# Performance work log

Hardware: AMD Instinct MI355X
Metric: run time of the kernel (lower is better)

## Reference

```python
import jax, jax.numpy as jnp
import numpy as np

N_NODES = 100000
N_EDGES = 3200000
D = 64


def setup_inputs() -> dict:
    key = jax.random.key(0)
    ks = jax.random.split(key, 8)
    x = jax.random.normal(ks[0], (N_NODES, D), dtype=jnp.float32)
    adj_row = jnp.sort(jax.random.randint(ks[1], (N_EDGES,), 0, N_NODES, dtype=jnp.int32)).astype(jnp.int64)
    adj_col = jax.random.randint(ks[2], (N_EDGES,), 0, N_NODES, dtype=jnp.int32).astype(jnp.int64)
    adj_val = jax.random.uniform(ks[3], (N_EDGES,), dtype=jnp.float32)
    stdv = 1.0 / np.sqrt(D)
    W1 = jax.random.uniform(ks[4], (D, D), minval=-stdv, maxval=stdv, dtype=jnp.float32)
    b1 = jax.random.uniform(ks[5], (D,), minval=-stdv, maxval=stdv, dtype=jnp.float32)
    W2 = jax.random.uniform(ks[6], (D, D), minval=-stdv, maxval=stdv, dtype=jnp.float32)
    b2 = jax.random.uniform(ks[7], (D,), minval=-stdv, maxval=stdv, dtype=jnp.float32)
    return {"x": x, "adj_row": adj_row, "adj_col": adj_col, "adj_val": adj_val,
            "W1": W1, "b1": b1, "W2": W2, "b2": b2}


def _spmm(row, col, val, support):
    # output[i] = sum_{e: row[e]==i} val[e] * support[col[e]]  (COO SpMM)
    return jax.ops.segment_sum(val[:, None] * support[col], row, num_segments=N_NODES)


def _gc_layer(x, row, col, val, W, b):
    support = x @ W            # dense mm [N, D]
    out = _spmm(row, col, val, support)
    return out + b


def reference(x, adj_row, adj_col, adj_val, W1, b1, W2, b2):
    # layer 0 + LeakyReLU(0.2)
    h = _gc_layer(x, adj_row, adj_col, adj_val, W1, b1)
    h = jnp.where(h >= 0, h, 0.2 * h)
    # dropout is identity in eval mode
    # layer 1 (no activation)
    out = _gc_layer(h, adj_row, adj_col, adj_val, W2, b2)
    return out
```

## Files before the change

kernel.cpp:

```cpp
#include <hip/hip_runtime.h>

#define NN 100000
#define NE 3200000
#define DD 64
#define KE 64
#define NW (NE / KE)
#define GEMM_BLOCKS 391
#define PREP_BLOCKS 12501

typedef unsigned int uint32;

__device__ inline uint32 bf16_rne(float f) {
    uint32 u = __float_as_uint(f);
    return (u + 0x7fffu + ((u >> 16) & 1u)) >> 16;
}

__global__ __launch_bounds__(256) void pre_kernel(
    const void* rowbuf, const void* colbuf, const float* __restrict__ val,
    const float* __restrict__ x, const float* __restrict__ W1,
    uint32* __restrict__ erec, int* __restrict__ rp, int* __restrict__ ws,
    uint32* __restrict__ xw) {
    __shared__ float4 sW[DD * 16];

    if (blockIdx.x < GEMM_BLOCKS) {
        for (int i = threadIdx.x; i < DD * 16; i += 256)
            sW[i] = ((const float4*)W1)[i];
        __syncthreads();

        int row = blockIdx.x * 256 + threadIdx.x;
        if (row >= NN) return;

        float acc[DD];
#pragma unroll
        for (int j = 0; j < DD; ++j) acc[j] = 0.f;

        const float4* Bp = (const float4*)(x + (size_t)row * DD);
#pragma unroll
        for (int k4 = 0; k4 < 16; ++k4) {
            float4 x4 = Bp[k4];
            float xs[4] = {x4.x, x4.y, x4.z, x4.w};
#pragma unroll
            for (int kk = 0; kk < 4; ++kk) {
                float xk = xs[kk];
                int k = 4 * k4 + kk;
#pragma unroll
                for (int j4 = 0; j4 < 16; ++j4) {
                    float4 w = sW[k * 16 + j4];
                    acc[4 * j4 + 0] = fmaf(xk, w.x, acc[4 * j4 + 0]);
                    acc[4 * j4 + 1] = fmaf(xk, w.y, acc[4 * j4 + 1]);
                    acc[4 * j4 + 2] = fmaf(xk, w.z, acc[4 * j4 + 2]);
                    acc[4 * j4 + 3] = fmaf(xk, w.w, acc[4 * j4 + 3]);
                }
            }
        }
        uint32* o = xw + (size_t)row * 32;
#pragma unroll
        for (int q = 0; q < 32; ++q)
            o[q] = bf16_rne(acc[2 * q]) | (bf16_rne(acc[2 * q + 1]) << 16);
        return;
    }

    int e = (blockIdx.x - GEMM_BLOCKS) * 256 + threadIdx.x;
    if (e >= NE + 32) return;
    if (e >= NE) { erec[e] = 0u; return; }

    const int* p32 = (const int*)rowbuf;
    bool is64 = (p32[NE / 2 + 1] == 0 && p32[NE / 2] != 0);

    int r, rn, c;
    if (is64) {
        const long long* row = (const long long*)rowbuf;
        const long long* col = (const long long*)colbuf;
        r  = (int)row[e];
        rn = (e == NE - 1) ? NN : (int)row[e + 1];
        c  = (int)col[e];
    } else {
        const int* row = (const int*)rowbuf;
        const int* col = (const int*)colbuf;
        r  = row[e];
        rn = (e == NE - 1) ? NN : row[e + 1];
        c  = col[e];
    }
    erec[e] = ((bf16_rne(val[e]) & 0x7fffu) << 17) | (uint32)c;
    for (int q = r + 1; q <= rn; ++q) rp[q] = e + 1;
    if (e == 0) {
        for (int q = 0; q <= r; ++q) rp[q] = 0;
        ws[0]  = 0;
        ws[NW] = NN;
    }
    if (((e + 1) & (KE - 1)) == 0 && (e + 1) < NE)
        ws[(e + 1) / KE] = r + 1;
}

#define ISSUE(G, U, I) {                                        \
    U = (uint32)__shfl((int)rw, (I), 16);                       \
    G = ((const uint2*)Xq)[((U & 0x1ffffu) << 4) + sl]; }

#define FLUSH() {                                                       \
    float y0 = a0 + bv.x, y1 = a1 + bv.y,                               \
          y2 = a2 + bv.z, y3 = a3 + bv.w;                               \
    if (L1) {                                                           \
        y0 = (y0 >= 0.f) ? y0 : 0.2f * y0;                              \
        y1 = (y1 >= 0.f) ? y1 : 0.2f * y1;                              \
        y2 = (y2 >= 0.f) ? y2 : 0.2f * y2;                              \
        y3 = (y3 >= 0.f) ? y3 : 0.2f * y3;                              \
        unsigned long long pk =                                         \
            (unsigned long long)(bf16_rne(y0) | (bf16_rne(y1) << 16)) | \
            ((unsigned long long)(bf16_rne(y2) | (bf16_rne(y3) << 16)) << 32); \
        __builtin_nontemporal_store(pk,                                 \
            (unsigned long long*)((uint2*)obv + (size_t)rr * 16 + sl)); \
    } else {                                                            \
        float* op = (float*)obv + (size_t)rr * 64 + sl * 4;             \
        __builtin_nontemporal_store(y0, op);                            \
        __builtin_nontemporal_store(y1, op + 1);                        \
        __builtin_nontemporal_store(y2, op + 2);                        \
        __builtin_nontemporal_store(y3, op + 3);                        \
    }                                                                   \
    a0 = 0.f; a1 = 0.f; a2 = 0.f; a3 = 0.f; ++rr; }

#define ACCUM(G, U, I) {                                        \
    while (e0 + (I) >= re) {                                    \
        FLUSH();                                                \
        re = (rr < r1) ? rp[rr + 1] : 0x7fffffff;               \
    }                                                           \
    float vi_ = __uint_as_float((U >> 17) << 16);               \
    a0 = fmaf(vi_, __uint_as_float(G.x << 16),          a0);    \
    a1 = fmaf(vi_, __uint_as_float(G.x & 0xffff0000u),  a1);    \
    a2 = fmaf(vi_, __uint_as_float(G.y << 16),          a2);    \
    a3 = fmaf(vi_, __uint_as_float(G.y & 0xffff0000u),  a3); }

template <bool L1>
__global__ __launch_bounds__(256) void spmm_kernel(
    const uint32* __restrict__ Xq, const uint32* __restrict__ erec,
    const int* __restrict__ rp, const int* __restrict__ ws,
    const float* __restrict__ bias, void* __restrict__ obv) {
    int worker = (blockIdx.x * blockDim.x + threadIdx.x) >> 4;
    int sl = threadIdx.x & 15;
    if (worker >= NW) return;

    int rr = ws[worker];
    int r1 = ws[worker + 1];
    if (rr >= r1) return;

    const float4 bv = ((const float4*)bias)[sl];

    int eb = rp[rr];
    int ee = rp[r1];
    int re = rp[rr + 1];
    float a0 = 0.f, a1 = 0.f, a2 = 0.f, a3 = 0.f;

    for (int e0 = eb; e0 < ee; e0 += 16) {
        uint32 rw = __builtin_nontemporal_load(&erec[e0 + sl]);
        rw = (e0 + sl < ee) ? rw : 0u;
        uint2  g0, g1, g2, g3, g4, g5, g6, g7;
        uint2  h0, h1, h2, h3, h4, h5, h6, h7;
        uint32 u0, u1, u2, u3, u4, u5, u6, u7;
        uint32 w0, w1, w2, w3, w4, w5, w6, w7;
        ISSUE(g0, u0, 0)  ISSUE(g1, u1, 1)  ISSUE(g2, u2, 2)  ISSUE(g3, u3, 3)
        ISSUE(g4, u4, 4)  ISSUE(g5, u5, 5)  ISSUE(g6, u6, 6)  ISSUE(g7, u7, 7)
        ISSUE(h0, w0, 8)  ISSUE(h1, w1, 9)  ISSUE(h2, w2, 10) ISSUE(h3, w3, 11)
        ISSUE(h4, w4, 12) ISSUE(h5, w5, 13) ISSUE(h6, w6, 14) ISSUE(h7, w7, 15)
        ACCUM(g0, u0, 0)  ACCUM(g1, u1, 1)  ACCUM(g2, u2, 2)  ACCUM(g3, u3, 3)
        ACCUM(g4, u4, 4)  ACCUM(g5, u5, 5)  ACCUM(g6, u6, 6)  ACCUM(g7, u7, 7)
        ACCUM(h0, w0, 8)  ACCUM(h1, w1, 9)  ACCUM(h2, w2, 10) ACCUM(h3, w3, 11)
        ACCUM(h4, w4, 12) ACCUM(h5, w5, 13) ACCUM(h6, w6, 14) ACCUM(h7, w7, 15)
    }
    while (rr < r1) { FLUSH(); }
}

__global__ __launch_bounds__(256) void gemm_bb_kernel(
    const uint32* __restrict__ Bb, const float* __restrict__ W,
    uint32* __restrict__ ob) {
    __shared__ float4 sW[DD * 16];
    for (int i = threadIdx.x; i < DD * 16; i += 256)
        sW[i] = ((const float4*)W)[i];
    __syncthreads();

    int row = blockIdx.x * 256 + threadIdx.x;
    if (row >= NN) return;

    float acc[DD];
#pragma unroll
    for (int j = 0; j < DD; ++j) acc[j] = 0.f;

    const uint4* Bp = (const uint4*)(Bb + (size_t)row * 32);
#pragma unroll
    for (int q4 = 0; q4 < 8; ++q4) {
        uint4 u4 = Bp[q4];
        uint32 us[4] = {u4.x, u4.y, u4.z, u4.w};
#pragma unroll
        for (int t = 0; t < 4; ++t) {
            int k = q4 * 8 + t * 2;
            float x0 = __uint_as_float(us[t] << 16);
            float x1 = __uint_as_float(us[t] & 0xffff0000u);
#pragma unroll
            for (int j4 = 0; j4 < 16; ++j4) {
                float4 w0 = sW[k * 16 + j4];
                float4 w1 = sW[(k + 1) * 16 + j4];
                acc[4 * j4 + 0] = fmaf(x0, w0.x, acc[4 * j4 + 0]);
                acc[4 * j4 + 1] = fmaf(x0, w0.y, acc[4 * j4 + 1]);
                acc[4 * j4 + 2] = fmaf(x0, w0.z, acc[4 * j4 + 2]);
                acc[4 * j4 + 3] = fmaf(x0, w0.w, acc[4 * j4 + 3]);
                acc[4 * j4 + 0] = fmaf(x1, w1.x, acc[4 * j4 + 0]);
                acc[4 * j4 + 1] = fmaf(x1, w1.y, acc[4 * j4 + 1]);
                acc[4 * j4 + 2] = fmaf(x1, w1.z, acc[4 * j4 + 2]);
                acc[4 * j4 + 3] = fmaf(x1, w1.w, acc[4 * j4 + 3]);
            }
        }
    }

    uint32* o = ob + (size_t)row * 32;
#pragma unroll
    for (int q = 0; q < 32; ++q)
        o[q] = bf16_rne(acc[2 * q]) | (bf16_rne(acc[2 * q + 1]) << 16);
}

extern "C" void kernel_launch(void* const* d_in, const int* in_sizes, int n_in,
                              void* d_out, int out_size, void* d_ws, size_t ws_size,
                              hipStream_t stream) {
    const float* x       = (const float*)d_in[0];
    const void*  adj_row = d_in[1];
    const void*  adj_col = d_in[2];
    const float* adj_val = (const float*)d_in[3];
    const float* W1      = (const float*)d_in[4];
    const float* b1      = (const float*)d_in[5];
    const float* W2      = (const float*)d_in[6];
    const float* b2      = (const float*)d_in[7];
    float*       out     = (float*)d_out;

    uint32* bufA = (uint32*)d_ws;
    uint32* bufB = bufA + (size_t)NN * 32;
    uint32* erec = bufB + (size_t)NN * 32;
    int*    rp   = (int*)(erec + NE + 32);
    int*    wst  = rp + (NN + 1);

    const int spmm_blocks = (NW * 16) / 256;

    pre_kernel<<<GEMM_BLOCKS + PREP_BLOCKS, 256, 0, stream>>>(
        adj_row, adj_col, adj_val, x, W1, erec, rp, wst, bufB);

    spmm_kernel<true><<<spmm_blocks, 256, 0, stream>>>(bufB, erec, rp, wst,
                                                       b1, bufA);

    gemm_bb_kernel<<<GEMM_BLOCKS, 256, 0, stream>>>(bufA, W2, bufB);

    spmm_kernel<false><<<spmm_blocks, 256, 0, stream>>>(bufB, erec, rp, wst,
                                                        b2, out);
}
```

Baseline: 222.3 us.

## Quantize gathered feature rows to int8 with per-row scale

Replaces the bf16 packed intermediate features with uint8 (offset-128) per-row quantized values plus a float scale per row. The SpMM gathers 64-byte rows and a scale, and corrects the offset via an accumulated sum of weights at flush. The intent is to halve the random gather traffic, which dominates the SpMM. In exchange it adds quantization error, an extra scale load per edge, and issues loads in two batches of eight instead of sixteen.

```diff
diff --git a/kernel.cpp b/kernel.cpp
--- a/kernel.cpp
+++ b/kernel.cpp
@@ -15,11 +15,30 @@
     return (u + 0x7fffu + ((u >> 16) & 1u)) >> 16;
 }
 
+__device__ inline void quant_store(const float* acc, uint32* __restrict__ qrow,
+                                   float* __restrict__ scp) {
+    float m = 0.f;
+#pragma unroll
+    for (int j = 0; j < DD; ++j) m = fmaxf(m, fabsf(acc[j]));
+    float inv = (m > 0.f) ? (127.f / m) : 0.f;
+    *scp = m * (1.f / 127.f);
+#pragma unroll
+    for (int q = 0; q < 16; ++q) {
+        uint32 p = 0;
+#pragma unroll
+        for (int b = 0; b < 4; ++b) {
+            int v = (int)rintf(acc[4 * q + b] * inv) + 128;
+            p |= ((uint32)v) << (8 * b);
+        }
+        qrow[q] = p;
+    }
+}
+
 __global__ __launch_bounds__(256) void pre_kernel(
     const void* rowbuf, const void* colbuf, const float* __restrict__ val,
     const float* __restrict__ x, const float* __restrict__ W1,
     uint32* __restrict__ erec, int* __restrict__ rp, int* __restrict__ ws,
-    uint32* __restrict__ xw) {
+    uint32* __restrict__ qt, float* __restrict__ sc) {
     __shared__ float4 sW[DD * 16];
 
     if (blockIdx.x < GEMM_BLOCKS) {
@@ -53,10 +72,7 @@
                 }
             }
         }
-        uint32* o = xw + (size_t)row * 32;
-#pragma unroll
-        for (int q = 0; q < 32; ++q)
-            o[q] = bf16_rne(acc[2 * q]) | (bf16_rne(acc[2 * q + 1]) << 16);
+        quant_store(acc, qt + (size_t)row * 16, sc + row);
         return;
     }
 
@@ -92,13 +108,17 @@
         ws[(e + 1) / KE] = r + 1;
 }
 
-#define ISSUE(G, U, I) {                                        \
-    U = (uint32)__shfl((int)rw, (I), 16);                       \
-    G = ((const uint2*)Xq)[((U & 0x1ffffu) << 4) + sl]; }
+#define ISSUE(G, S, V, I) {                                     \
+    uint32 t_ = (uint32)__shfl((int)rw, (I), 16);               \
+    uint32 c_ = t_ & 0x1ffffu;                                  \
+    G = qt[((size_t)c_ << 4) + (uint32)sl];                     \
+    S = sc[c_];                                                 \
+    V = __uint_as_float((t_ >> 17) << 16); }
 
 #define FLUSH() {                                                       \
-    float y0 = a0 + bv.x, y1 = a1 + bv.y,                               \
-          y2 = a2 + bv.z, y3 = a3 + bv.w;                               \
+    float cr_ = fmaf(-128.f, ts, 0.f);                                  \
+    float y0 = a0 + cr_ + bv.x, y1 = a1 + cr_ + bv.y,                   \
+          y2 = a2 + cr_ + bv.z, y3 = a3 + cr_ + bv.w;                   \
     if (L1) {                                                           \
         y0 = (y0 >= 0.f) ? y0 : 0.2f * y0;                              \
         y1 = (y1 >= 0.f) ? y1 : 0.2f * y1;                              \
@@ -116,24 +136,26 @@
         __builtin_nontemporal_store(y2, op + 2);                        \
         __builtin_nontemporal_store(y3, op + 3);                        \
     }                                                                   \
-    a0 = 0.f; a1 = 0.f; a2 = 0.f; a3 = 0.f; ++rr; }
-
-#define ACCUM(G, U, I) {                                        \
+    a0 = 0.f; a1 = 0.f; a2 = 0.f; a3 = 0.f; ts = 0.f; ++rr; }
+
+#define ACCUM(G, S, V, I) {                                     \
     while (e0 + (I) >= re) {                                    \
         FLUSH();                                                \
         re = (rr < r1) ? rp[rr + 1] : 0x7fffffff;               \
     }                                                           \
-    float vi_ = __uint_as_float((U >> 17) << 16);               \
-    a0 = fmaf(vi_, __uint_as_float(G.x << 16),          a0);    \
-    a1 = fmaf(vi_, __uint_as_float(G.x & 0xffff0000u),  a1);    \
-    a2 = fmaf(vi_, __uint_as_float(G.y << 16),          a2);    \
-    a3 = fmaf(vi_, __uint_as_float(G.y & 0xffff0000u),  a3); }
+    float t_ = V * S;                                           \
+    a0 = fmaf(t_, (float)(G & 0xffu),         a0);              \
+    a1 = fmaf(t_, (float)((G >> 8) & 0xffu),  a1);              \
+    a2 = fmaf(t_, (float)((G >> 16) & 0xffu), a2);              \
+    a3 = fmaf(t_, (float)(G >> 24),           a3);              \
+    ts += t_; }
 
 template <bool L1>
 __global__ __launch_bounds__(256) void spmm_kernel(
-    const uint32* __restrict__ Xq, const uint32* __restrict__ erec,
-    const int* __restrict__ rp, const int* __restrict__ ws,
-    const float* __restrict__ bias, void* __restrict__ obv) {
+    const uint32* __restrict__ qt, const float* __restrict__ sc,
+    const uint32* __restrict__ erec, const int* __restrict__ rp,
+    const int* __restrict__ ws, const float* __restrict__ bias,
+    void* __restrict__ obv) {
     int worker = (blockIdx.x * blockDim.x + threadIdx.x) >> 4;
     int sl = threadIdx.x & 15;
     if (worker >= NW) return;
@@ -147,30 +169,37 @@
     int eb = rp[rr];
     int ee = rp[r1];
     int re = rp[rr + 1];
-    float a0 = 0.f, a1 = 0.f, a2 = 0.f, a3 = 0.f;
+    float a0 = 0.f, a1 = 0.f, a2 = 0.f, a3 = 0.f, ts = 0.f;
 
     for (int e0 = eb; e0 < ee; e0 += 16) {
         uint32 rw = __builtin_nontemporal_load(&erec[e0 + sl]);
         rw = (e0 + sl < ee) ? rw : 0u;
-        uint2  g0, g1, g2, g3, g4, g5, g6, g7;
-        uint2  h0, h1, h2, h3, h4, h5, h6, h7;
-        uint32 u0, u1, u2, u3, u4, u5, u6, u7;
-        uint32 w0, w1, w2, w3, w4, w5, w6, w7;
-        ISSUE(g0, u0, 0)  ISSUE(g1, u1, 1)  ISSUE(g2, u2, 2)  ISSUE(g3, u3, 3)
-        ISSUE(g4, u4, 4)  ISSUE(g5, u5, 5)  ISSUE(g6, u6, 6)  ISSUE(g7, u7, 7)
-        ISSUE(h0, w0, 8)  ISSUE(h1, w1, 9)  ISSUE(h2, w2, 10) ISSUE(h3, w3, 11)
-        ISSUE(h4, w4, 12) ISSUE(h5, w5, 13) ISSUE(h6, w6, 14) ISSUE(h7, w7, 15)
-        ACCUM(g0, u0, 0)  ACCUM(g1, u1, 1)  ACCUM(g2, u2, 2)  ACCUM(g3, u3, 3)
-        ACCUM(g4, u4, 4)  ACCUM(g5, u5, 5)  ACCUM(g6, u6, 6)  ACCUM(g7, u7, 7)
-        ACCUM(h0, w0, 8)  ACCUM(h1, w1, 9)  ACCUM(h2, w2, 10) ACCUM(h3, w3, 11)
-        ACCUM(h4, w4, 12) ACCUM(h5, w5, 13) ACCUM(h6, w6, 14) ACCUM(h7, w7, 15)
+        uint32 g0, g1, g2, g3, g4, g5, g6, g7;
+        float  s0, s1, s2, s3, s4, s5, s6, s7;
+        float  v0, v1, v2, v3, v4, v5, v6, v7;
+        ISSUE(g0, s0, v0, 0)  ISSUE(g1, s1, v1, 1)
+        ISSUE(g2, s2, v2, 2)  ISSUE(g3, s3, v3, 3)
+        ISSUE(g4, s4, v4, 4)  ISSUE(g5, s5, v5, 5)
+        ISSUE(g6, s6, v6, 6)  ISSUE(g7, s7, v7, 7)
+        ACCUM(g0, s0, v0, 0)  ACCUM(g1, s1, v1, 1)
+        ACCUM(g2, s2, v2, 2)  ACCUM(g3, s3, v3, 3)
+        ACCUM(g4, s4, v4, 4)  ACCUM(g5, s5, v5, 5)
+        ACCUM(g6, s6, v6, 6)  ACCUM(g7, s7, v7, 7)
+        ISSUE(g0, s0, v0, 8)  ISSUE(g1, s1, v1, 9)
+        ISSUE(g2, s2, v2, 10) ISSUE(g3, s3, v3, 11)
+        ISSUE(g4, s4, v4, 12) ISSUE(g5, s5, v5, 13)
+        ISSUE(g6, s6, v6, 14) ISSUE(g7, s7, v7, 15)
+        ACCUM(g0, s0, v0, 8)  ACCUM(g1, s1, v1, 9)
+        ACCUM(g2, s2, v2, 10) ACCUM(g3, s3, v3, 11)
+        ACCUM(g4, s4, v4, 12) ACCUM(g5, s5, v5, 13)
+        ACCUM(g6, s6, v6, 14) ACCUM(g7, s7, v7, 15)
     }
     while (rr < r1) { FLUSH(); }
 }
 
 __global__ __launch_bounds__(256) void gemm_bb_kernel(
     const uint32* __restrict__ Bb, const float* __restrict__ W,
-    uint32* __restrict__ ob) {
+    uint32* __restrict__ qt, float* __restrict__ sc) {
     __shared__ float4 sW[DD * 16];
     for (int i = threadIdx.x; i < DD * 16; i += 256)
         sW[i] = ((const float4*)W)[i];
@@ -208,11 +237,7 @@
             }
         }
     }
-
-    uint32* o = ob + (size_t)row * 32;
-#pragma unroll
-    for (int q = 0; q < 32; ++q)
-        o[q] = bf16_rne(acc[2 * q]) | (bf16_rne(acc[2 * q + 1]) << 16);
+    quant_store(acc, qt + (size_t)row * 16, sc + row);
 }
 
 extern "C" void kernel_launch(void* const* d_in, const int* in_sizes, int n_in,
@@ -229,21 +254,22 @@
     float*       out     = (float*)d_out;
 
     uint32* bufA = (uint32*)d_ws;
-    uint32* bufB = bufA + (size_t)NN * 32;
-    uint32* erec = bufB + (size_t)NN * 32;
+    uint32* qt   = bufA + (size_t)NN * 32;
+    float*  sc   = (float*)(qt + (size_t)NN * 16);
+    uint32* erec = (uint32*)(sc + NN);
     int*    rp   = (int*)(erec + NE + 32);
     int*    wst  = rp + (NN + 1);
 
     const int spmm_blocks = (NW * 16) / 256;
 
     pre_kernel<<<GEMM_BLOCKS + PREP_BLOCKS, 256, 0, stream>>>(
-        adj_row, adj_col, adj_val, x, W1, erec, rp, wst, bufB);
-
-    spmm_kernel<true><<<spmm_blocks, 256, 0, stream>>>(bufB, erec, rp, wst,
+        adj_row, adj_col, adj_val, x, W1, erec, rp, wst, qt, sc);
+
+    spmm_kernel<true><<<spmm_blocks, 256, 0, stream>>>(qt, sc, erec, rp, wst,
                                                        b1, bufA);
 
-    gemm_bb_kernel<<<GEMM_BLOCKS, 256, 0, stream>>>(bufA, W2, bufB);
-
-    spmm_kernel<false><<<spmm_blocks, 256, 0, stream>>>(bufB, erec, rp, wst,
+    gemm_bb_kernel<<<GEMM_BLOCKS, 256, 0, stream>>>(bufA, W2, qt, sc);
+
+    spmm_kernel<false><<<spmm_blocks, 256, 0, stream>>>(qt, sc, erec, rp, wst,
                                                         b2, out);
 }
```

Result: faster. 185.6 us (-16.5%).
